# Optimization experiments

Hardware: AMD Instinct MI355X
Metric: run time of the kernel (lower is better)

Reference implementation:

```python
import jax, jax.numpy as jnp
import numpy as np

SCORE_THR = 0.05
NMS_THR = 0.5
PRE_NMS_K = 512  # fixed pre-NMS candidate count for static shapes
IMG = 1024.0


def _corners(boxes):
    # boxes: (..., 5) = (cx, cy, w, h, angle_deg) -> (..., 4, 2) CCW corners
    cx, cy, w, h, a = (boxes[..., i] for i in range(5))
    t = a * (np.pi / 180.0)
    c, s = jnp.cos(t), jnp.sin(t)
    dx, dy = w * 0.5, h * 0.5
    lx = jnp.stack([-dx, dx, dx, -dx], axis=-1)
    ly = jnp.stack([-dy, -dy, dy, dy], axis=-1)
    px = cx[..., None] + c[..., None] * lx - s[..., None] * ly
    py = cy[..., None] + s[..., None] * lx + c[..., None] * ly
    return jnp.stack([px, py], axis=-1)


def _clip(pts, cnt, a, b):
    # Sutherland-Hodgman clip of polygons pts (P,C,2) with vertex counts cnt (P,)
    # against half-plane left of directed edge a->b (each (P,2)).
    P, C, _ = pts.shape
    idx = jnp.arange(C)
    valid = idx[None, :] < cnt[:, None]
    nxt_idx = jnp.where(idx[None, :] + 1 >= cnt[:, None], 0, idx[None, :] + 1)
    nxt = jnp.take_along_axis(pts, jnp.broadcast_to(nxt_idx[:, :, None], pts.shape), axis=1)
    e = b - a
    d_cur = e[:, None, 0] * (pts[..., 1] - a[:, None, 1]) - e[:, None, 1] * (pts[..., 0] - a[:, None, 0])
    d_nxt = e[:, None, 0] * (nxt[..., 1] - a[:, None, 1]) - e[:, None, 1] * (nxt[..., 0] - a[:, None, 0])
    cur_in = d_cur >= 0.0
    nxt_in = d_nxt >= 0.0
    denom = d_cur - d_nxt
    t = d_cur / jnp.where(jnp.abs(denom) < 1e-9, 1e-9, denom)
    ipt = pts + t[..., None] * (nxt - pts)
    emit_cur = cur_in & valid
    emit_int = (cur_in ^ nxt_in) & valid
    em_pts = jnp.stack([pts, ipt], axis=2).reshape(P, 2 * C, 2)
    em_flag = jnp.stack([emit_cur, emit_int], axis=2).reshape(P, 2 * C)
    pos = jnp.cumsum(em_flag.astype(jnp.int32), axis=1) - 1
    tgt = jnp.where(em_flag, pos, C)  # dump slot C for non-emitted
    out = jnp.zeros((P, C + 1, 2), pts.dtype)
    out = out.at[jnp.arange(P)[:, None], tgt].set(jnp.where(em_flag[..., None], em_pts, 0.0))
    return out[:, :C], em_flag.sum(axis=1).astype(jnp.int32)


def _poly_area(pts, cnt):
    P, C, _ = pts.shape
    idx = jnp.arange(C)
    valid = idx[None, :] < cnt[:, None]
    nxt_idx = jnp.where(idx[None, :] + 1 >= cnt[:, None], 0, idx[None, :] + 1)
    nxt = jnp.take_along_axis(pts, jnp.broadcast_to(nxt_idx[:, :, None], pts.shape), axis=1)
    cr = pts[..., 0] * nxt[..., 1] - pts[..., 1] * nxt[..., 0]
    area = 0.5 * jnp.sum(jnp.where(valid, cr, 0.0), axis=1)
    return jnp.where(cnt >= 3, jnp.abs(area), 0.0)


def _rotated_iou(boxes):
    # boxes: (K,5) -> exact oriented IoU matrix (K,K) via convex polygon clipping
    K = boxes.shape[0]
    corners = _corners(boxes)  # (K,4,2)
    areas = boxes[:, 2] * boxes[:, 3]
    ca = jnp.broadcast_to(corners[:, None], (K, K, 4, 2)).reshape(K * K, 4, 2)
    cb = jnp.broadcast_to(corners[None, :], (K, K, 4, 2)).reshape(K * K, 4, 2)
    pts = jnp.concatenate([ca, jnp.zeros((K * K, 4, 2), ca.dtype)], axis=1)  # capacity 8
    cnt = jnp.full((K * K,), 4, jnp.int32)
    for e in range(4):
        pts, cnt = _clip(pts, cnt, cb[:, e], cb[:, (e + 1) % 4])
    inter = _poly_area(pts, cnt).reshape(K, K)
    union = areas[:, None] + areas[None, :] - inter
    return inter / jnp.maximum(union, 1e-6)


def _decode(anchors, deltas):
    # anchors/deltas: (N,5). Standard rotated delta decode.
    ax, ay, aw, ah, aa = (anchors[:, i] for i in range(5))
    dx, dy, dw, dh, da = (deltas[:, i] for i in range(5))
    px = ax + dx * aw
    py = ay + dy * ah
    pw = aw * jnp.exp(jnp.clip(dw, -4.0, 4.0))
    ph = ah * jnp.exp(jnp.clip(dh, -4.0, 4.0))
    pa = aa + da * (180.0 / np.pi)  # radian delta -> degrees
    return jnp.stack([px, py, pw, ph, pa], axis=1)


def _per_image(logits, deltas, anchors):
    scores = jax.nn.sigmoid(logits)            # (N, C)
    max_scores = jnp.max(scores, axis=1)       # (N,)
    labels = jnp.argmax(scores, axis=1)
    boxes = _decode(anchors, deltas)           # (N, 5)
    top_s, top_i = jax.lax.top_k(max_scores, PRE_NMS_K)
    tb = boxes[top_i]
    tl = labels[top_i]
    valid = top_s > SCORE_THR
    iou = jax.lax.stop_gradient(_rotated_iou(tb))  # (K, K)
    rng = jnp.arange(PRE_NMS_K)
    def body(i, keep):
        sup = keep[i] & (iou[i] > NMS_THR) & (rng > i)
        return keep & (~sup)
    keep = jax.lax.fori_loop(0, PRE_NMS_K, body, valid)
    return tb, top_s, tl, keep


def setup_inputs() -> dict:
    key = jax.random.key(0)
    k1, k2, k3 = jax.random.split(key, 3)
    B, N, C = 4, 392832, 15
    # shift logits so sigmoid scores straddle the 0.05 threshold (sparse positives)
    cls_logits = jax.random.normal(k1, (B, N, C), jnp.float32) * 1.5 - 4.0
    box_regression = jax.random.normal(k2, (B, N, 5), jnp.float32) * 0.1
    u = jax.random.uniform(k3, (N, 5), jnp.float32)
    anchors = jnp.stack([u[:, 0] * IMG, u[:, 1] * IMG,
                         16.0 + u[:, 2] * 240.0, 16.0 + u[:, 3] * 240.0,
                         (u[:, 4] - 0.5) * 180.0], axis=1)
    return {"cls_logits": cls_logits, "box_regression": box_regression, "anchors": anchors}


def reference(cls_logits, box_regression, anchors):
    boxes, scores, labels, keep = jax.vmap(_per_image, in_axes=(0, 0, None))(
        cls_logits, box_regression, anchors)
    # (B,K,5) boxes, (B,K) scores (descending), (B,K) labels, (B,K) keep mask from rotated NMS
    return boxes, scores, labels, keep
```

## Files before the change

kernel.cpp:

```cpp
#include <hip/hip_runtime.h>
#include <hip/hip_bf16.h>
#include <stdint.h>

typedef unsigned int u32;
typedef unsigned long long u64;

#define K_SEL 512
#define NBINS 4096
#define CAP 8192
#define SCORE_THR 0.05f
#define NMS_THR 0.5f
#define RPB 3072
#define SLABS 128

__device__ __forceinline__ u32 fkey(float x) {
  u32 u = __float_as_uint(x);
  return u ^ ((u32)((int)u >> 31) | 0x80000000u);
}
__device__ __forceinline__ float fkey_inv(u32 k) {
  u32 u = (k & 0x80000000u) ? (k ^ 0x80000000u) : ~k;
  return __uint_as_float(u);
}

__global__ __launch_bounds__(256) void k_maxhist(
    const float* __restrict__ logits, u32* __restrict__ skey,
    u32* __restrict__ histp, float4* __restrict__ zbuf, int nz4, int N) {
  int blk = blockIdx.x;
  int b = blk >> 7;
  int lb = blk & (SLABS - 1);
  for (int i = blk * 256 + threadIdx.x; i < nz4; i += gridDim.x * 256)
    zbuf[i] = make_float4(0.f, 0.f, 0.f, 0.f);
  __shared__ __align__(16) float tile[256 * 15];
  __shared__ u32 sh[NBINS];
  for (int i = threadIdx.x; i < NBINS; i += 256) sh[i] = 0;
  int r0 = lb * RPB;
  for (int c = 0; c < RPB / 256; c++) {
    int n0 = r0 + c * 256;
    if (n0 >= N) break;
    int nrow = min(256, N - n0);
    const float* src = logits + ((size_t)b * N + n0) * 15;
    int tot = nrow * 15;
    if (((tot & 3) == 0) && ((((size_t)src) & 15) == 0)) {
      const float4* s4 = (const float4*)src;
      float4* t4 = (float4*)tile;
      int n4 = tot >> 2;
      for (int i = threadIdx.x; i < n4; i += 256) t4[i] = s4[i];
    } else {
      for (int i = threadIdx.x; i < tot; i += 256) tile[i] = src[i];
    }
    __syncthreads();
    if (threadIdx.x < nrow) {
      const float* row = tile + threadIdx.x * 15;
      float mv = row[0];
      for (int cc = 1; cc < 15; cc++) mv = fmaxf(mv, row[cc]);
      u32 key = fkey(mv);
      skey[(size_t)b * N + n0 + threadIdx.x] = key;
      atomicAdd(&sh[key >> 20], 1u);
    }
    __syncthreads();
  }
  u32* hp = histp + (size_t)blk * NBINS;
  for (int i = threadIdx.x; i < NBINS; i += 256) hp[i] = sh[i];
}

__global__ __launch_bounds__(256) void k_slabred(const u32* __restrict__ histp,
                                                 u32* __restrict__ hred) {
  int b = blockIdx.y;
  int bin = blockIdx.x * 256 + threadIdx.x;
  const u32* base = histp + (size_t)b * SLABS * NBINS + bin;
  u32 s = 0;
#pragma unroll 8
  for (int sl = 0; sl < SLABS; sl++) s += base[(size_t)sl * NBINS];
  hred[b * NBINS + bin] = s;
}

__global__ __launch_bounds__(256) void k_cutoff(const u32* __restrict__ hred,
                                                u32* __restrict__ cutT) {
  int b = blockIdx.x;
  int t = threadIdx.x;
  const u32* hb = hred + b * NBINS;
  u32 h[16];
  u32 s = 0;
#pragma unroll
  for (int i = 0; i < 16; i++) {
    h[i] = hb[t * 16 + i];
    s += h[i];
  }
  __shared__ u32 cs[256];
  cs[t] = s;
  __syncthreads();
  for (int off = 1; off < 256; off <<= 1) {
    u32 add = (t + off < 256) ? cs[t + off] : 0;
    __syncthreads();
    cs[t] += add;
    __syncthreads();
  }
  u32 run = (t < 255) ? cs[t + 1] : 0;
  for (int i = 15; i >= 0; i--) {
    u32 sfx = run + h[i];
    if (run < (u32)K_SEL && sfx >= (u32)K_SEL) cutT[b] = (u32)(t * 16 + i);
    run = sfx;
  }
}

__global__ __launch_bounds__(256) void k_compact(
    const u32* __restrict__ skey, const u32* __restrict__ cutT,
    u64* __restrict__ cand, u32* __restrict__ cnt, int N) {
  int b = blockIdx.y;
  int n = blockIdx.x * 256 + threadIdx.x;
  __shared__ u32 lcnt, lbase;
  if (threadIdx.x == 0) lcnt = 0;
  __syncthreads();
  u32 key = 0;
  bool ok = false;
  u32 lpos = 0;
  if (n < N) {
    key = skey[(size_t)b * N + n];
    ok = (key >> 20) >= cutT[b];
  }
  if (ok) lpos = atomicAdd(&lcnt, 1u);
  __syncthreads();
  if (threadIdx.x == 0 && lcnt) lbase = atomicAdd(&cnt[b * 32], lcnt);
  __syncthreads();
  if (ok) {
    u32 pos = lbase + lpos;
    if (pos < CAP)
      cand[(size_t)b * CAP + pos] = ((u64)key << 32) | (u32)(~(u32)n);
  }
}

__global__ __launch_bounds__(256) void k_rankdecode(
    const u64* __restrict__ cand, const u32* __restrict__ cnt,
    const float* __restrict__ logits, const float* __restrict__ deltas,
    const float* __restrict__ anchors, float* __restrict__ out,
    float* __restrict__ corners, float4* __restrict__ meta,
    u64* __restrict__ validw, int N, int C, int off_scores, int off_labels) {
  int b = blockIdx.y;
  int M = (int)min(cnt[b * 32], (u32)CAP);
  if (blockIdx.x * 256 >= (u32)M) return;
  int m = blockIdx.x * 256 + threadIdx.x;
  u64 my = (m < M) ? cand[(size_t)b * CAP + m] : 0ull;
  int rank = 0;
  __shared__ u64 t[256];
  for (int j0 = 0; j0 < M; j0 += 256) {
    int j = j0 + threadIdx.x;
    t[threadIdx.x] = (j < M) ? cand[(size_t)b * CAP + j] : 0ull;
    __syncthreads();
    int lim = min(256, M - j0);
    for (int jj = 0; jj < lim; jj++) rank += (t[jj] > my) ? 1 : 0;
    __syncthreads();
  }
  if (m >= M || rank >= K_SEL) return;
  int g = b * K_SEL + rank;
  u32 key = (u32)(my >> 32);
  int idx = (int)(~(u32)my);
  float ml = fkey_inv(key);
  float score = 1.0f / (1.0f + expf(-ml));
  const float* lr = logits + ((size_t)b * N + idx) * C;
  float bv = lr[0];
  int lab = 0;
  for (int c = 1; c < C; c++) {
    float v = lr[c];
    if (v > bv) { bv = v; lab = c; }
  }
  const float* ar = anchors + (size_t)idx * 5;
  const float* dr = deltas + ((size_t)b * N + idx) * 5;
  float ax = ar[0], ay = ar[1], aw = ar[2], ah = ar[3], aa = ar[4];
  float dx = dr[0], dy = dr[1], dwv = dr[2], dhv = dr[3], da = dr[4];
  float px = ax + dx * aw;
  float py = ay + dy * ah;
  float pw = aw * expf(fminf(fmaxf(dwv, -4.0f), 4.0f));
  float ph = ah * expf(fminf(fmaxf(dhv, -4.0f), 4.0f));
  float pa = aa + da * 57.295779513082323f;
  float* ob = out + (size_t)g * 5;
  ob[0] = px; ob[1] = py; ob[2] = pw; ob[3] = ph; ob[4] = pa;
  out[off_scores + g] = score;
  out[off_labels + g] = (float)lab;
  if (score > SCORE_THR) atomicOr(&validw[g >> 6], 1ull << (g & 63));
  float tt = pa * 0.017453292519943295f;
  float cc = cosf(tt), sn = sinf(tt);
  float hx = pw * 0.5f, hy = ph * 0.5f;
  float* cp = corners + (size_t)g * 8;
  cp[0] = px + cc * (-hx) - sn * (-hy);
  cp[1] = py + sn * (-hx) + cc * (-hy);
  cp[2] = px + cc * (hx) - sn * (-hy);
  cp[3] = py + sn * (hx) + cc * (-hy);
  cp[4] = px + cc * (hx) - sn * (hy);
  cp[5] = py + sn * (hx) + cc * (hy);
  cp[6] = px + cc * (-hx) - sn * (hy);
  cp[7] = py + sn * (-hx) + cc * (hy);
  meta[g] = make_float4(px, py, 0.5f * sqrtf(pw * pw + ph * ph), pw * ph);
}

__global__ __launch_bounds__(256) void k_pairclip(
    const float4* __restrict__ meta, const float* __restrict__ corners,
    u64* __restrict__ sup) {
  int b = blockIdx.x >> 7;
  int i0 = (blockIdx.x & 127) * 4;
  __shared__ float js_x[K_SEL], js_y[K_SEL], js_r[K_SEL], js_a[K_SEL];
  __shared__ u32 list[2048];
  __shared__ u32 lcnt;
  if (threadIdx.x == 0) lcnt = 0;
  for (int t = threadIdx.x; t < K_SEL; t += 256) {
    float4 mj = meta[b * K_SEL + t];
    js_x[t] = mj.x; js_y[t] = mj.y; js_r[t] = mj.z; js_a[t] = mj.w;
  }
  __syncthreads();
  int i = i0 + (threadIdx.x >> 6);
  int lane = threadIdx.x & 63;
  float4 mi = meta[b * K_SEL + i];
  float cxi = mi.x, cyi = mi.y, ri = mi.z, ai = mi.w;
#pragma unroll
  for (int k = 0; k < 8; k++) {
    int j = lane + 64 * k;
    if (j <= i) continue;
    float ddx = cxi - js_x[j], ddy = cyi - js_y[j];
    float rr = ri + js_r[j];
    float d2 = ddx * ddx + ddy * ddy;
    if (d2 > rr * rr * 1.0001f) continue;
    float aj = js_a[j];
    float mnA = fminf(ai, aj), mxA = fmaxf(ai, aj);
    if (2.0f * mnA < 0.999f * mxA) continue;
    u32 p = atomicAdd(&lcnt, 1u);
    list[p] = ((u32)i << 9) | (u32)j;
  }
  __syncthreads();
  u32 M = lcnt;
  for (u32 l = threadIdx.x; l < M; l += 256) {
    u32 pk = list[l];
    int i2 = (int)(pk >> 9);
    int j2 = (int)(pk & 511u);
    int gi2 = b * K_SEL + i2, gj2 = b * K_SEL + j2;
    const float* ci = corners + (size_t)gi2 * 8;
    const float* cj = corners + (size_t)gj2 * 8;
    float X[8], Y[8], bx[4], by[4];
#pragma unroll
    for (int m = 0; m < 4; m++) {
      X[m] = ci[2 * m]; Y[m] = ci[2 * m + 1];
      X[m + 4] = 0.f; Y[m + 4] = 0.f;
      bx[m] = cj[2 * m]; by[m] = cj[2 * m + 1];
    }
    int cnt = 4;
#pragma unroll
    for (int e = 0; e < 4; e++) {
      float axp = bx[e], ayp = by[e];
      float ex = bx[(e + 1) & 3] - axp, ey = by[(e + 1) & 3] - ayp;
      float d[8];
#pragma unroll
      for (int m = 0; m < 8; m++)
        d[m] = ex * (Y[m] - ayp) - ey * (X[m] - axp);
      float NX[8], NY[8];
#pragma unroll
      for (int s = 0; s < 8; s++) { NX[s] = 0.f; NY[s] = 0.f; }
      int oc = 0;
#pragma unroll
      for (int m = 0; m < 8; m++) {
        bool act = (m < cnt);
        bool isLast = (m + 1 == cnt);
        float dn = isLast ? d[0] : d[(m + 1) & 7];
        float xn = isLast ? X[0] : X[(m + 1) & 7];
        float yn = isLast ? Y[0] : Y[(m + 1) & 7];
        bool cin = (d[m] >= 0.f), nin = (dn >= 0.f);
        bool e1 = act && cin;
        bool e2 = act && (cin != nin);
#pragma unroll
        for (int s = 0; s < 8; s++) {
          bool w = e1 && (oc == s);
          NX[s] = w ? X[m] : NX[s];
          NY[s] = w ? Y[m] : NY[s];
        }
        oc += e1 ? 1 : 0;
        float den = d[m] - dn;
        float dd = (fabsf(den) < 1e-9f) ? 1e-9f : den;
        float tt = d[m] / dd;
        float ix = X[m] + tt * (xn - X[m]);
        float iy = Y[m] + tt * (yn - Y[m]);
#pragma unroll
        for (int s = 0; s < 8; s++) {
          bool w = e2 && (oc == s);
          NX[s] = w ? ix : NX[s];
          NY[s] = w ? iy : NY[s];
        }
        oc += e2 ? 1 : 0;
      }
      cnt = oc;
#pragma unroll
      for (int m = 0; m < 8; m++) { X[m] = NX[m]; Y[m] = NY[m]; }
    }
    float sum = 0.f;
#pragma unroll
    for (int m = 0; m < 8; m++) {
      bool act = (m < cnt);
      bool isLast = (m + 1 == cnt);
      float xn = isLast ? X[0] : X[(m + 1) & 7];
      float yn = isLast ? Y[0] : Y[(m + 1) & 7];
      float cr = X[m] * yn - Y[m] * xn;
      sum += act ? cr : 0.f;
    }
    float inter = (cnt >= 3) ? 0.5f * fabsf(sum) : 0.f;
    float ai2 = js_a[i2], aj2 = js_a[j2];
    float uni = ai2 + aj2 - inter;
    float iou = inter / fmaxf(uni, 1e-6f);
    if (iou > NMS_THR)
      atomicOr(&sup[((size_t)b * K_SEL + i2) * 8 + (j2 >> 6)],
               1ull << (j2 & 63));
  }
}

#define NSTEP(PB, S, cc)                                                   \
  {                                                                        \
    u64 live_ = ((vv >> (S)) & ~(rw >> (S))) & 1ull;                       \
    u64 m_ = (u64)0 - live_;                                               \
    rw |= PB & m_;                                                         \
    km |= live_ << (S);                                                    \
    if ((S) < 48) PB = lsn[((cc)*64 + (S) + 16) * 8 + (cc)];               \
  }

#define NGROUP16(S0, cc)                                                   \
  NSTEP(P0, (S0) + 0, cc) NSTEP(P1, (S0) + 1, cc)                          \
  NSTEP(P2, (S0) + 2, cc) NSTEP(P3, (S0) + 3, cc)                          \
  NSTEP(P4, (S0) + 4, cc) NSTEP(P5, (S0) + 5, cc)                          \
  NSTEP(P6, (S0) + 6, cc) NSTEP(P7, (S0) + 7, cc)                          \
  NSTEP(P8, (S0) + 8, cc) NSTEP(P9, (S0) + 9, cc)                          \
  NSTEP(P10, (S0) + 10, cc) NSTEP(P11, (S0) + 11, cc)                      \
  NSTEP(P12, (S0) + 12, cc) NSTEP(P13, (S0) + 13, cc)                      \
  NSTEP(P14, (S0) + 14, cc) NSTEP(P15, (S0) + 15, cc)

#define NCHUNK(cc)                                                         \
  {                                                                        \
    u64 vv = vsh[cc];                                                      \
    u64 rw = rem[cc];                                                      \
    u64 km = 0;                                                            \
    u64 P0 = lsn[((cc)*64 + 0) * 8 + (cc)];                                \
    u64 P1 = lsn[((cc)*64 + 1) * 8 + (cc)];                                \
    u64 P2 = lsn[((cc)*64 + 2) * 8 + (cc)];                                \
    u64 P3 = lsn[((cc)*64 + 3) * 8 + (cc)];                                \
    u64 P4 = lsn[((cc)*64 + 4) * 8 + (cc)];                                \
    u64 P5 = lsn[((cc)*64 + 5) * 8 + (cc)];                                \
    u64 P6 = lsn[((cc)*64 + 6) * 8 + (cc)];                                \
    u64 P7 = lsn[((cc)*64 + 7) * 8 + (cc)];                                \
    u64 P8 = lsn[((cc)*64 + 8) * 8 + (cc)];                                \
    u64 P9 = lsn[((cc)*64 + 9) * 8 + (cc)];                                \
    u64 P10 = lsn[((cc)*64 + 10) * 8 + (cc)];                              \
    u64 P11 = lsn[((cc)*64 + 11) * 8 + (cc)];                              \
    u64 P12 = lsn[((cc)*64 + 12) * 8 + (cc)];                              \
    u64 P13 = lsn[((cc)*64 + 13) * 8 + (cc)];                              \
    u64 P14 = lsn[((cc)*64 + 14) * 8 + (cc)];                              \
    u64 P15 = lsn[((cc)*64 + 15) * 8 + (cc)];                              \
    NGROUP16(0, cc) NGROUP16(16, cc) NGROUP16(32, cc) NGROUP16(48, cc)     \
    u64 kk = km;                                                           \
    while (kk) {                                                           \
      int r_ = (cc)*64 + __builtin_ctzll(kk);                              \
      kk &= kk - 1ull;                                                     \
      const u64* rb_ = lsn + r_ * 8;                                       \
      rem[0] |= rb_[0]; rem[1] |= rb_[1]; rem[2] |= rb_[2];                \
      rem[3] |= rb_[3]; rem[4] |= rb_[4]; rem[5] |= rb_[5];                \
      rem[6] |= rb_[6]; rem[7] |= rb_[7];                                  \
    }                                                                      \
    ko[(cc)*64 + lane] = (float)((km >> lane) & 1ull);                     \
  }

__global__ __launch_bounds__(256) void k_nms(const u64* __restrict__ sup,
                                             const u64* __restrict__ validw,
                                             float* __restrict__ keep_out) {
  int b = blockIdx.x;
  __shared__ __align__(16) u64 lsn[K_SEL * 8];
  __shared__ u64 vsh[8];
  const u64* sb = sup + (size_t)b * K_SEL * 8;
  {
    const ulonglong2* s2 = (const ulonglong2*)sb;
    ulonglong2* l2 = (ulonglong2*)lsn;
    for (int k = threadIdx.x; k < K_SEL * 4; k += 256) l2[k] = s2[k];
  }
  if (threadIdx.x < 8) vsh[threadIdx.x] = validw[b * 8 + threadIdx.x];
  __syncthreads();
  if (threadIdx.x >= 64) return;
  int lane = threadIdx.x;
  u64 rem[8] = {0, 0, 0, 0, 0, 0, 0, 0};
  float* ko = keep_out + b * K_SEL;
  NCHUNK(0)
  NCHUNK(1)
  NCHUNK(2)
  NCHUNK(3)
  NCHUNK(4)
  NCHUNK(5)
  NCHUNK(6)
  NCHUNK(7)
}

extern "C" void kernel_launch(void* const* d_in, const int* in_sizes, int n_in,
                              void* d_out, int out_size, void* d_ws,
                              size_t ws_size, hipStream_t stream) {
  const float* logits = (const float*)d_in[0];
  const float* deltas = (const float*)d_in[1];
  const float* anchors = (const float*)d_in[2];
  float* out = (float*)d_out;
  int N = in_sizes[2] / 5;
  int B = in_sizes[1] / (N * 5);
  int C = (int)((long long)in_sizes[0] / ((long long)B * N));
  int BK = B * K_SEL;

  char* ws = (char*)d_ws;
  size_t o_cnt = 0;
  size_t o_vw = o_cnt + 512;
  size_t o_sup = o_vw + 256;
  size_t zero_end = o_sup + (size_t)B * K_SEL * 8 * 8;
  size_t o_cut = (zero_end + 255) & ~(size_t)255;
  size_t o_skey = (o_cut + 256 + 255) & ~(size_t)255;
  size_t o_cand = (o_skey + (size_t)B * N * 4 + 255) & ~(size_t)255;
  size_t o_corn = (o_cand + (size_t)B * CAP * 8 + 255) & ~(size_t)255;
  size_t o_meta = (o_corn + (size_t)BK * 8 * 4 + 255) & ~(size_t)255;
  size_t o_hp = (o_meta + (size_t)BK * 16 + 255) & ~(size_t)255;
  size_t o_hred = (o_hp + (size_t)B * SLABS * NBINS * 4 + 255) & ~(size_t)255;

  u32* cnt = (u32*)(ws + o_cnt);
  u64* validw = (u64*)(ws + o_vw);
  u64* sup = (u64*)(ws + o_sup);
  u32* cutT = (u32*)(ws + o_cut);
  u32* skey = (u32*)(ws + o_skey);
  u64* cand = (u64*)(ws + o_cand);
  float* corners = (float*)(ws + o_corn);
  float4* meta = (float4*)(ws + o_meta);
  u32* histp = (u32*)(ws + o_hp);
  u32* hred = (u32*)(ws + o_hred);

  int nz4 = (int)(zero_end >> 4);

  int nb = (N + 255) / 256;
  k_maxhist<<<B * SLABS, 256, 0, stream>>>(logits, skey, histp, (float4*)ws,
                                           nz4, N);
  k_slabred<<<dim3(NBINS / 256, B), 256, 0, stream>>>(histp, hred);
  k_cutoff<<<B, 256, 0, stream>>>(hred, cutT);
  k_compact<<<dim3(nb, B), 256, 0, stream>>>(skey, cutT, cand, cnt, N);
  int off_scores = BK * 5, off_labels = BK * 6, off_keep = BK * 7;
  k_rankdecode<<<dim3(CAP / 256, B), 256, 0, stream>>>(
      cand, cnt, logits, deltas, anchors, out, corners, meta, validw, N, C,
      off_scores, off_labels);
  k_pairclip<<<B * 128, 256, 0, stream>>>(meta, corners, sup);
  k_nms<<<B, 256, 0, stream>>>(sup, validw, out + off_keep);
}
```

Measured before the change: 121.2 us.

## Fuse slab reduction with cutoff and pair clipping with NMS via last-block counters

Merges the histogram slab-reduce and cutoff kernels, and the pairwise rotated-IoU kernel and the greedy NMS kernel, into single launches. In each, the last block to finish per image, found with an atomic counter in zeroed workspace, performs the dependent serial stage. This removes two kernel launches and their inter-kernel gaps. In exchange it adds threadfences, atomic reads of global data, and a larger shared-memory footprint for the pair-clip blocks, which could reduce occupancy.

After: 153.4 us. 26.5% more time.

```diff
diff --git a/kernel.cpp b/kernel.cpp
--- a/kernel.cpp
+++ b/kernel.cpp
@@ -63,31 +63,33 @@
   for (int i = threadIdx.x; i < NBINS; i += 256) hp[i] = sh[i];
 }
 
-__global__ __launch_bounds__(256) void k_slabred(const u32* __restrict__ histp,
-                                                 u32* __restrict__ hred) {
-  int b = blockIdx.y;
-  int bin = blockIdx.x * 256 + threadIdx.x;
+__global__ __launch_bounds__(256) void k_slabredcut(
+    const u32* __restrict__ histp, u32* __restrict__ hred,
+    u32* __restrict__ done3, u32* __restrict__ cutT) {
+  int b = blockIdx.x >> 4;
+  int part = blockIdx.x & 15;
+  int bin = part * 256 + threadIdx.x;
   const u32* base = histp + (size_t)b * SLABS * NBINS + bin;
   u32 s = 0;
 #pragma unroll 8
   for (int sl = 0; sl < SLABS; sl++) s += base[(size_t)sl * NBINS];
   hred[b * NBINS + bin] = s;
-}
-
-__global__ __launch_bounds__(256) void k_cutoff(const u32* __restrict__ hred,
-                                                u32* __restrict__ cutT) {
-  int b = blockIdx.x;
+  __threadfence();
+  __shared__ u32 lastflag;
+  if (threadIdx.x == 0) lastflag = atomicAdd(&done3[b * 32], 1u);
+  __syncthreads();
+  if (lastflag != 15) return;
   int t = threadIdx.x;
-  const u32* hb = hred + b * NBINS;
+  u32* hb = hred + b * NBINS;
   u32 h[16];
-  u32 s = 0;
+  u32 sum = 0;
 #pragma unroll
   for (int i = 0; i < 16; i++) {
-    h[i] = hb[t * 16 + i];
-    s += h[i];
+    h[i] = atomicOr(&hb[t * 16 + i], 0u);
+    sum += h[i];
   }
   __shared__ u32 cs[256];
-  cs[t] = s;
+  cs[t] = sum;
   __syncthreads();
   for (int off = 1; off < 256; off <<= 1) {
     u32 add = (t + off < 256) ? cs[t + off] : 0;
@@ -190,121 +192,6 @@
   cp[6] = px + cc * (-hx) - sn * (hy);
   cp[7] = py + sn * (-hx) + cc * (hy);
   meta[g] = make_float4(px, py, 0.5f * sqrtf(pw * pw + ph * ph), pw * ph);
-}
-
-__global__ __launch_bounds__(256) void k_pairclip(
-    const float4* __restrict__ meta, const float* __restrict__ corners,
-    u64* __restrict__ sup) {
-  int b = blockIdx.x >> 7;
-  int i0 = (blockIdx.x & 127) * 4;
-  __shared__ float js_x[K_SEL], js_y[K_SEL], js_r[K_SEL], js_a[K_SEL];
-  __shared__ u32 list[2048];
-  __shared__ u32 lcnt;
-  if (threadIdx.x == 0) lcnt = 0;
-  for (int t = threadIdx.x; t < K_SEL; t += 256) {
-    float4 mj = meta[b * K_SEL + t];
-    js_x[t] = mj.x; js_y[t] = mj.y; js_r[t] = mj.z; js_a[t] = mj.w;
-  }
-  __syncthreads();
-  int i = i0 + (threadIdx.x >> 6);
-  int lane = threadIdx.x & 63;
-  float4 mi = meta[b * K_SEL + i];
-  float cxi = mi.x, cyi = mi.y, ri = mi.z, ai = mi.w;
-#pragma unroll
-  for (int k = 0; k < 8; k++) {
-    int j = lane + 64 * k;
-    if (j <= i) continue;
-    float ddx = cxi - js_x[j], ddy = cyi - js_y[j];
-    float rr = ri + js_r[j];
-    float d2 = ddx * ddx + ddy * ddy;
-    if (d2 > rr * rr * 1.0001f) continue;
-    float aj = js_a[j];
-    float mnA = fminf(ai, aj), mxA = fmaxf(ai, aj);
-    if (2.0f * mnA < 0.999f * mxA) continue;
-    u32 p = atomicAdd(&lcnt, 1u);
-    list[p] = ((u32)i << 9) | (u32)j;
-  }
-  __syncthreads();
-  u32 M = lcnt;
-  for (u32 l = threadIdx.x; l < M; l += 256) {
-    u32 pk = list[l];
-    int i2 = (int)(pk >> 9);
-    int j2 = (int)(pk & 511u);
-    int gi2 = b * K_SEL + i2, gj2 = b * K_SEL + j2;
-    const float* ci = corners + (size_t)gi2 * 8;
-    const float* cj = corners + (size_t)gj2 * 8;
-    float X[8], Y[8], bx[4], by[4];
-#pragma unroll
-    for (int m = 0; m < 4; m++) {
-      X[m] = ci[2 * m]; Y[m] = ci[2 * m + 1];
-      X[m + 4] = 0.f; Y[m + 4] = 0.f;
-      bx[m] = cj[2 * m]; by[m] = cj[2 * m + 1];
-    }
-    int cnt = 4;
-#pragma unroll
-    for (int e = 0; e < 4; e++) {
-      float axp = bx[e], ayp = by[e];
-      float ex = bx[(e + 1) & 3] - axp, ey = by[(e + 1) & 3] - ayp;
-      float d[8];
-#pragma unroll
-      for (int m = 0; m < 8; m++)
-        d[m] = ex * (Y[m] - ayp) - ey * (X[m] - axp);
-      float NX[8], NY[8];
-#pragma unroll
-      for (int s = 0; s < 8; s++) { NX[s] = 0.f; NY[s] = 0.f; }
-      int oc = 0;
-#pragma unroll
-      for (int m = 0; m < 8; m++) {
-        bool act = (m < cnt);
-        bool isLast = (m + 1 == cnt);
-        float dn = isLast ? d[0] : d[(m + 1) & 7];
-        float xn = isLast ? X[0] : X[(m + 1) & 7];
-        float yn = isLast ? Y[0] : Y[(m + 1) & 7];
-        bool cin = (d[m] >= 0.f), nin = (dn >= 0.f);
-        bool e1 = act && cin;
-        bool e2 = act && (cin != nin);
-#pragma unroll
-        for (int s = 0; s < 8; s++) {
-          bool w = e1 && (oc == s);
-          NX[s] = w ? X[m] : NX[s];
-          NY[s] = w ? Y[m] : NY[s];
-        }
-        oc += e1 ? 1 : 0;
-        float den = d[m] - dn;
-        float dd = (fabsf(den) < 1e-9f) ? 1e-9f : den;
-        float tt = d[m] / dd;
-        float ix = X[m] + tt * (xn - X[m]);
-        float iy = Y[m] + tt * (yn - Y[m]);
-#pragma unroll
-        for (int s = 0; s < 8; s++) {
-          bool w = e2 && (oc == s);
-          NX[s] = w ? ix : NX[s];
-          NY[s] = w ? iy : NY[s];
-        }
-        oc += e2 ? 1 : 0;
-      }
-      cnt = oc;
-#pragma unroll
-      for (int m = 0; m < 8; m++) { X[m] = NX[m]; Y[m] = NY[m]; }
-    }
-    float sum = 0.f;
-#pragma unroll
-    for (int m = 0; m < 8; m++) {
-      bool act = (m < cnt);
-      bool isLast = (m + 1 == cnt);
-      float xn = isLast ? X[0] : X[(m + 1) & 7];
-      float yn = isLast ? Y[0] : Y[(m + 1) & 7];
-      float cr = X[m] * yn - Y[m] * xn;
-      sum += act ? cr : 0.f;
-    }
-    float inter = (cnt >= 3) ? 0.5f * fabsf(sum) : 0.f;
-    float ai2 = js_a[i2], aj2 = js_a[j2];
-    float uni = ai2 + aj2 - inter;
-    float iou = inter / fmaxf(uni, 1e-6f);
-    if (iou > NMS_THR)
-      atomicOr(&sup[((size_t)b * K_SEL + i2) * 8 + (j2 >> 6)],
-               1ull << (j2 & 63));
-  }
 }
 
 #define NSTEP(PB, S, cc)                                                   \
@@ -360,32 +247,152 @@
     ko[(cc)*64 + lane] = (float)((km >> lane) & 1ull);                     \
   }
 
-__global__ __launch_bounds__(256) void k_nms(const u64* __restrict__ sup,
-                                             const u64* __restrict__ validw,
-                                             float* __restrict__ keep_out) {
-  int b = blockIdx.x;
-  __shared__ __align__(16) u64 lsn[K_SEL * 8];
+__global__ __launch_bounds__(256) void k_pairclipnms(
+    const float4* __restrict__ meta, const float* __restrict__ corners,
+    u64* __restrict__ sup, const u64* __restrict__ validw,
+    u32* __restrict__ done2, float* __restrict__ keep_out) {
+  __shared__ __align__(16) char smem[33024];
+  float* js_x = (float*)smem;
+  float* js_y = (float*)(smem + 2048);
+  float* js_r = (float*)(smem + 4096);
+  float* js_a = (float*)(smem + 6144);
+  u32* list = (u32*)(smem + 8192);
+  u32* lcnt = (u32*)(smem + 16384);
+  int b = blockIdx.x >> 7;
+  int i0 = (blockIdx.x & 127) * 4;
+  if (threadIdx.x == 0) *lcnt = 0;
+  for (int t = threadIdx.x; t < K_SEL; t += 256) {
+    float4 mj = meta[b * K_SEL + t];
+    js_x[t] = mj.x; js_y[t] = mj.y; js_r[t] = mj.z; js_a[t] = mj.w;
+  }
+  __syncthreads();
+  int i = i0 + (threadIdx.x >> 6);
+  int lane = threadIdx.x & 63;
+  float4 mi = meta[b * K_SEL + i];
+  float cxi = mi.x, cyi = mi.y, ri = mi.z, ai = mi.w;
+#pragma unroll
+  for (int k = 0; k < 8; k++) {
+    int j = lane + 64 * k;
+    if (j <= i) continue;
+    float ddx = cxi - js_x[j], ddy = cyi - js_y[j];
+    float rr = ri + js_r[j];
+    float d2 = ddx * ddx + ddy * ddy;
+    if (d2 > rr * rr * 1.0001f) continue;
+    float aj = js_a[j];
+    float mnA = fminf(ai, aj), mxA = fmaxf(ai, aj);
+    if (2.0f * mnA < 0.999f * mxA) continue;
+    u32 p = atomicAdd(lcnt, 1u);
+    list[p] = ((u32)i << 9) | (u32)j;
+  }
+  __syncthreads();
+  u32 M = *lcnt;
+  for (u32 l = threadIdx.x; l < M; l += 256) {
+    u32 pk = list[l];
+    int i2 = (int)(pk >> 9);
+    int j2 = (int)(pk & 511u);
+    int gi2 = b * K_SEL + i2, gj2 = b * K_SEL + j2;
+    const float* ci = corners + (size_t)gi2 * 8;
+    const float* cj = corners + (size_t)gj2 * 8;
+    float X[8], Y[8], bx[4], by[4];
+#pragma unroll
+    for (int m = 0; m < 4; m++) {
+      X[m] = ci[2 * m]; Y[m] = ci[2 * m + 1];
+      X[m + 4] = 0.f; Y[m + 4] = 0.f;
+      bx[m] = cj[2 * m]; by[m] = cj[2 * m + 1];
+    }
+    int cnt2 = 4;
+#pragma unroll
+    for (int e = 0; e < 4; e++) {
+      float axp = bx[e], ayp = by[e];
+      float ex = bx[(e + 1) & 3] - axp, ey = by[(e + 1) & 3] - ayp;
+      float d[8];
+#pragma unroll
+      for (int m = 0; m < 8; m++)
+        d[m] = ex * (Y[m] - ayp) - ey * (X[m] - axp);
+      float NX[8], NY[8];
+#pragma unroll
+      for (int s = 0; s < 8; s++) { NX[s] = 0.f; NY[s] = 0.f; }
+      int oc = 0;
+#pragma unroll
+      for (int m = 0; m < 8; m++) {
+        bool act = (m < cnt2);
+        bool isLast = (m + 1 == cnt2);
+        float dn = isLast ? d[0] : d[(m + 1) & 7];
+        float xn = isLast ? X[0] : X[(m + 1) & 7];
+        float yn = isLast ? Y[0] : Y[(m + 1) & 7];
+        bool cin = (d[m] >= 0.f), nin = (dn >= 0.f);
+        bool e1 = act && cin;
+        bool e2 = act && (cin != nin);
+#pragma unroll
+        for (int s = 0; s < 8; s++) {
+          bool w = e1 && (oc == s);
+          NX[s] = w ? X[m] : NX[s];
+          NY[s] = w ? Y[m] : NY[s];
+        }
+        oc += e1 ? 1 : 0;
+        float den = d[m] - dn;
+        float dd = (fabsf(den) < 1e-9f) ? 1e-9f : den;
+        float tt = d[m] / dd;
+        float ix = X[m] + tt * (xn - X[m]);
+        float iy = Y[m] + tt * (yn - Y[m]);
+#pragma unroll
+        for (int s = 0; s < 8; s++) {
+          bool w = e2 && (oc == s);
+          NX[s] = w ? ix : NX[s];
+          NY[s] = w ? iy : NY[s];
+        }
+        oc += e2 ? 1 : 0;
+      }
+      cnt2 = oc;
+#pragma unroll
+      for (int m = 0; m < 8; m++) { X[m] = NX[m]; Y[m] = NY[m]; }
+    }
+    float sum = 0.f;
+#pragma unroll
+    for (int m = 0; m < 8; m++) {
+      bool act = (m < cnt2);
+      bool isLast = (m + 1 == cnt2);
+      float xn = isLast ? X[0] : X[(m + 1) & 7];
+      float yn = isLast ? Y[0] : Y[(m + 1) & 7];
+      float cr = X[m] * yn - Y[m] * xn;
+      sum += act ? cr : 0.f;
+    }
+    float inter = (cnt2 >= 3) ? 0.5f * fabsf(sum) : 0.f;
+    float ai2 = js_a[i2], aj2 = js_a[j2];
+    float uni = ai2 + aj2 - inter;
+    float iou = inter / fmaxf(uni, 1e-6f);
+    if (iou > NMS_THR)
+      atomicOr(&sup[((size_t)b * K_SEL + i2) * 8 + (j2 >> 6)],
+               1ull << (j2 & 63));
+  }
+  __syncthreads();
+  __threadfence();
+  __shared__ u32 lastflag;
+  if (threadIdx.x == 0) lastflag = atomicAdd(&done2[b * 32], 1u);
+  __syncthreads();
+  if (lastflag != 127) return;
+  u64* lsn = (u64*)smem;
   __shared__ u64 vsh[8];
-  const u64* sb = sup + (size_t)b * K_SEL * 8;
+  u64* sb = sup + (size_t)b * K_SEL * 8;
+  for (int k2 = threadIdx.x; k2 < K_SEL * 8; k2 += 256)
+    lsn[k2] = atomicOr(&sb[k2], 0ull);
+  if (threadIdx.x < 8) vsh[threadIdx.x] = validw[b * 8 + threadIdx.x];
+  __syncthreads();
+  if (threadIdx.x >= 64) return;
+  int lane2 = threadIdx.x;
   {
-    const ulonglong2* s2 = (const ulonglong2*)sb;
-    ulonglong2* l2 = (ulonglong2*)lsn;
-    for (int k = threadIdx.x; k < K_SEL * 4; k += 256) l2[k] = s2[k];
-  }
-  if (threadIdx.x < 8) vsh[threadIdx.x] = validw[b * 8 + threadIdx.x];
-  __syncthreads();
-  if (threadIdx.x >= 64) return;
-  int lane = threadIdx.x;
-  u64 rem[8] = {0, 0, 0, 0, 0, 0, 0, 0};
-  float* ko = keep_out + b * K_SEL;
-  NCHUNK(0)
-  NCHUNK(1)
-  NCHUNK(2)
-  NCHUNK(3)
-  NCHUNK(4)
-  NCHUNK(5)
-  NCHUNK(6)
-  NCHUNK(7)
+    int lane = lane2;
+    u64 rem[8] = {0, 0, 0, 0, 0, 0, 0, 0};
+    float* ko = keep_out + b * K_SEL;
+    NCHUNK(0)
+    NCHUNK(1)
+    NCHUNK(2)
+    NCHUNK(3)
+    NCHUNK(4)
+    NCHUNK(5)
+    NCHUNK(6)
+    NCHUNK(7)
+  }
 }
 
 extern "C" void kernel_launch(void* const* d_in, const int* in_sizes, int n_in,
@@ -402,7 +409,9 @@
 
   char* ws = (char*)d_ws;
   size_t o_cnt = 0;
-  size_t o_vw = o_cnt + 512;
+  size_t o_done2 = o_cnt + 512;
+  size_t o_done3 = o_done2 + 512;
+  size_t o_vw = o_done3 + 512;
   size_t o_sup = o_vw + 256;
   size_t zero_end = o_sup + (size_t)B * K_SEL * 8 * 8;
   size_t o_cut = (zero_end + 255) & ~(size_t)255;
@@ -414,6 +423,8 @@
   size_t o_hred = (o_hp + (size_t)B * SLABS * NBINS * 4 + 255) & ~(size_t)255;
 
   u32* cnt = (u32*)(ws + o_cnt);
+  u32* done2 = (u32*)(ws + o_done2);
+  u32* done3 = (u32*)(ws + o_done3);
   u64* validw = (u64*)(ws + o_vw);
   u64* sup = (u64*)(ws + o_sup);
   u32* cutT = (u32*)(ws + o_cut);
@@ -429,13 +440,13 @@
   int nb = (N + 255) / 256;
   k_maxhist<<<B * SLABS, 256, 0, stream>>>(logits, skey, histp, (float4*)ws,
                                            nz4, N);
-  k_slabred<<<dim3(NBINS / 256, B), 256, 0, stream>>>(histp, hred);
-  k_cutoff<<<B, 256, 0, stream>>>(hred, cutT);
+  k_slabredcut<<<B * (NBINS / 256), 256, 0, stream>>>(histp, hred, done3,
+                                                      cutT);
   k_compact<<<dim3(nb, B), 256, 0, stream>>>(skey, cutT, cand, cnt, N);
   int off_scores = BK * 5, off_labels = BK * 6, off_keep = BK * 7;
   k_rankdecode<<<dim3(CAP / 256, B), 256, 0, stream>>>(
       cand, cnt, logits, deltas, anchors, out, corners, meta, validw, N, C,
       off_scores, off_labels);
-  k_pairclip<<<B * 128, 256, 0, stream>>>(meta, corners, sup);
-  k_nms<<<B, 256, 0, stream>>>(sup, validw, out + off_keep);
-}
+  k_pairclipnms<<<B * 128, 256, 0, stream>>>(meta, corners, sup, validw,
+                                             done2, out + off_keep);
+}
```
